# Kernel tuning notes

Measured on AMD Instinct MI355X. Metric: run time of the kernel, lower is better.

Reference implementation:

```python
import jax, jax.numpy as jnp
import numpy as np

H = 8   # heads
C = 64  # per-head channels (gnn_hidden_dim)
HID = H * C  # 512
IN_CH = 6
EMB = 64
U, M = 16, 512
N_NODES = U * M  # 8192
N_EDGES = 131072


def _tconv(x, src, dst, Wq, bq, Wk, bk, Wv, bv, Ws, bs):
    """PyG TransformerConv (concat=True, root_weight=True, beta=False, eval mode)."""
    N = x.shape[0]
    q = (x @ Wq + bq).reshape(N, H, C)
    k = (x @ Wk + bk).reshape(N, H, C)
    v = (x @ Wv + bv).reshape(N, H, C)
    # per-edge attention scores: query at dst (target i), key at src (source j)
    score = jnp.einsum('ehc,ehc->eh', q[dst], k[src]) / jnp.sqrt(jnp.float32(C))
    # segment softmax over incoming edges of each dst node
    mx = jax.ops.segment_max(score, dst, num_segments=N)
    ex = jnp.exp(score - mx[dst])
    denom = jax.ops.segment_sum(ex, dst, num_segments=N)
    alpha = ex / (denom[dst] + 1e-16)  # [E, H]
    msg = alpha[..., None] * v[src]    # [E, H, C]
    out = jax.ops.segment_sum(msg, dst, num_segments=N).reshape(N, HID)
    return out + x @ Ws + bs  # root/skip connection


def setup_inputs() -> dict:
    key = jax.random.key(0)
    ks = iter(jax.random.split(key, 64))
    s = 0.05

    def lin(k, i, o):
        k1, k2 = jax.random.split(k)
        return (jax.random.normal(k1, (i, o), jnp.float32) * s,
                jax.random.normal(k2, (o,), jnp.float32) * s)

    inp = {}
    inp['mission_coords'] = jax.random.uniform(next(ks), (M, 2), jnp.float32)
    inp['uavs_info'] = jax.random.uniform(next(ks), (U, 2), jnp.float32)
    inp['speeds'] = jax.random.uniform(next(ks), (U,), jnp.float32)
    inp['dist_matrix'] = jax.random.uniform(next(ks), (U, M), jnp.float32)
    inp['timetogo_matrix'] = jax.random.uniform(next(ks), (U, M), jnp.float32)
    inp['action_mask'] = jax.random.randint(next(ks), (U, M), 0, 2, jnp.int32)
    inp['edge_index'] = jax.random.randint(next(ks), (2, N_EDGES), 0, N_NODES, jnp.int64)
    inp['batch'] = jnp.zeros((U,), jnp.int64)

    # layer 0 (in=6)
    inp['Wq0'], inp['bq0'] = lin(next(ks), IN_CH, HID)
    inp['Wk0'], inp['bk0'] = lin(next(ks), IN_CH, HID)
    inp['Wv0'], inp['bv0'] = lin(next(ks), IN_CH, HID)
    inp['Ws0'], inp['bs0'] = lin(next(ks), IN_CH, HID)
    # layers 1..3 stacked (in=512)
    for nm in ['Wq', 'Wk', 'Wv', 'Ws']:
        Ws_, bs_ = [], []
        for _ in range(3):
            w, b = lin(next(ks), HID, HID)
            Ws_.append(w); bs_.append(b)
        inp[nm] = jnp.stack(Ws_)
        inp['b' + nm[1:].lower()] = jnp.stack(bs_)
    inp['Wout'], inp['bout'] = lin(next(ks), HID, EMB)
    inp['Wa1'], inp['ba1'] = lin(next(ks), EMB + 3, 128)
    inp['Wa2'], inp['ba2'] = lin(next(ks), 128, 1)
    inp['Wc1'], inp['bc1'] = lin(next(ks), EMB + 3, 128)
    inp['Wc2'], inp['bc2'] = lin(next(ks), 128, 1)
    return inp


def reference(mission_coords, uavs_info, speeds, dist_matrix, timetogo_matrix,
              action_mask, edge_index, batch,
              Wq0, bq0, Wk0, bk0, Wv0, bv0, Ws0, bs0,
              Wq, bq, Wk, bk, Wv, bv, Ws, bs,
              Wout, bout, Wa1, ba1, Wa2, ba2, Wc1, bc1, Wc2, bc2):
    u, m = uavs_info.shape[0], mission_coords.shape[0]
    mc = jnp.broadcast_to(mission_coords[None], (u, m, 2))
    mask_e = action_mask[..., None].astype(jnp.float32)
    sp_e = jnp.broadcast_to(speeds[:, None, None], (u, m, 1))
    x = jnp.concatenate([mc, mask_e, sp_e, dist_matrix[..., None],
                         timetogo_matrix[..., None]], axis=-1).reshape(u * m, IN_CH)
    src, dst = edge_index[0], edge_index[1]
    x = jax.nn.relu(_tconv(x, src, dst, Wq0, bq0, Wk0, bk0, Wv0, bv0, Ws0, bs0))
    for l in range(3):
        x = jax.nn.relu(_tconv(x, src, dst, Wq[l], bq[l], Wk[l], bk[l],
                               Wv[l], bv[l], Ws[l], bs[l]))
    x = x @ Wout + bout  # [U*M, EMB]
    uav_emb = x.reshape(u, m, EMB).sum(axis=1)  # sum pooling over missions
    combined = jnp.concatenate([uavs_info, uav_emb, speeds[:, None]], axis=-1)
    logits = jax.nn.relu(combined @ Wa1 + ba1) @ Wa2 + ba2  # [U, 1]
    action_probs = jax.nn.softmax(logits, axis=-1)
    state_values = (jax.nn.relu(combined @ Wc1 + bc1) @ Wc2 + bc2).squeeze()
    return action_probs, state_values
```

## Files before the change

kernel.cpp:

```cpp
#include <hip/hip_runtime.h>
#include <hip/hip_bf16.h>
#include <math.h>

#define NNODES 8192
#define NEDGES 131072
#define HID    512
#define UU     16
#define MM     512
#define NQKVS  2048

#if __has_builtin(__builtin_amdgcn_cvt_pk_f32_fp8) && __has_builtin(__builtin_amdgcn_cvt_pk_fp8_f32)
#define HAVE_FP8 1
#else
#define HAVE_FP8 0
#endif

#define KSCALE 16.0f
#define KISCALE (0.125f / 16.0f)

typedef __attribute__((ext_vector_type(8))) short bf16x8;
typedef __attribute__((ext_vector_type(4))) float f32x4;
typedef __attribute__((ext_vector_type(2))) float f32x2;

__device__ __forceinline__ float bf2f(ushort u) {
    return __uint_as_float(((unsigned)u) << 16);
}
__device__ __forceinline__ ushort f2bf(float f) {
    unsigned x = __float_as_uint(f);
    return (ushort)((x + 0x7fffu + ((x >> 16) & 1u)) >> 16);
}

__global__ __launch_bounds__(256) void k_build_x(
    const float* __restrict__ mc, const float* __restrict__ speeds,
    const float* __restrict__ dist, const float* __restrict__ ttg,
    const int* __restrict__ mask, float* __restrict__ x6)
{
    int n = blockIdx.x * blockDim.x + threadIdx.x;
    if (n >= NNODES) return;
    int u = n >> 9, m = n & 511;
    float* o = x6 + (size_t)n * 6;
    o[0] = mc[m * 2 + 0];
    o[1] = mc[m * 2 + 1];
    o[2] = (float)mask[u * MM + m];
    o[3] = speeds[u];
    o[4] = dist[u * MM + m];
    o[5] = ttg[u * MM + m];
}

__global__ __launch_bounds__(256) void k_wt(
    const float* __restrict__ Wq, const float* __restrict__ Wk,
    const float* __restrict__ Wv, const float* __restrict__ Ws,
    ushort* __restrict__ Wt)
{
    __shared__ float tile[64][65];
    int z = blockIdx.z;
    int l = z >> 2, which = z & 3;
    const float* src = (which == 0 ? Wq : which == 1 ? Wk : which == 2 ? Wv : Ws)
                       + (size_t)l * HID * HID;
    int k0 = blockIdx.x * 64, c0 = blockIdx.y * 64;
    int t = threadIdx.x;
#pragma unroll
    for (int i = 0; i < 16; ++i) {
        int idx = i * 256 + t;
        int r = idx >> 6, c = idx & 63;
        tile[r][c] = src[(size_t)(k0 + r) * HID + c0 + c];
    }
    __syncthreads();
    ushort* dst = Wt + ((size_t)l * NQKVS + which * HID + c0) * HID + k0;
#pragma unroll
    for (int i = 0; i < 16; ++i) {
        int idx = i * 256 + t;
        int r = idx >> 6, c = idx & 63;
        dst[(size_t)r * HID + c] = f2bf(tile[c][r]);
    }
}

__global__ __launch_bounds__(256) void k_bias(
    const float* __restrict__ bq, const float* __restrict__ bk,
    const float* __restrict__ bv, const float* __restrict__ bs,
    float* __restrict__ bcat)
{
    int i = blockIdx.x * 256 + threadIdx.x;
    int l = i >> 11, j = i & 2047;
    int which = j >> 9, jj = j & 511;
    const float* b = which == 0 ? bq : which == 1 ? bk : which == 2 ? bv : bs;
    bcat[i] = b[l * HID + jj];
}

__global__ __launch_bounds__(256) void k_lin0(
    const float* __restrict__ x6,
    const float* __restrict__ Wq0, const float* __restrict__ bq0,
    const float* __restrict__ Wk0, const float* __restrict__ bk0,
    const float* __restrict__ Wv0, const float* __restrict__ bv0,
    const float* __restrict__ Ws0, const float* __restrict__ bs0,
    ushort* __restrict__ Y, unsigned char* __restrict__ Kf8)
{
    int n = blockIdx.x;
    int j = threadIdx.x;
    int col0 = j * 8;
    int which = col0 >> 9, jj = col0 & 511;
    const float* W = which == 0 ? Wq0 : which == 1 ? Wk0 : which == 2 ? Wv0 : Ws0;
    const float* b = which == 0 ? bq0 : which == 1 ? bk0 : which == 2 ? bv0 : bs0;
    const float* xr = x6 + (size_t)n * 6;
    float x[6];
#pragma unroll
    for (int t = 0; t < 6; ++t) x[t] = xr[t];
    float s[8];
#pragma unroll
    for (int u = 0; u < 8; ++u) s[u] = b[jj + u];
#pragma unroll
    for (int t = 0; t < 6; ++t)
#pragma unroll
        for (int u = 0; u < 8; ++u)
            s[u] = fmaf(x[t], W[t * HID + jj + u], s[u]);
    bf16x8 o8;
#pragma unroll
    for (int u = 0; u < 8; ++u) o8[u] = (short)f2bf(s[u]);
    *(bf16x8*)(Y + (size_t)n * NQKVS + col0) = o8;
#if HAVE_FP8
    if (which == 1) {
        int w0 = __builtin_amdgcn_cvt_pk_fp8_f32(s[0] * KSCALE, s[1] * KSCALE, 0, false);
        w0     = __builtin_amdgcn_cvt_pk_fp8_f32(s[2] * KSCALE, s[3] * KSCALE, w0, true);
        int w1 = __builtin_amdgcn_cvt_pk_fp8_f32(s[4] * KSCALE, s[5] * KSCALE, 0, false);
        w1     = __builtin_amdgcn_cvt_pk_fp8_f32(s[6] * KSCALE, s[7] * KSCALE, w1, true);
        uint2 uu; uu.x = (unsigned)w0; uu.y = (unsigned)w1;
        *(uint2*)(Kf8 + (size_t)n * HID + jj) = uu;
    }
#endif
}

#define GBM 128
#define GBN 128
#define GBK 64
#define TILEB (GBM * GBK * 2)
#define BUFB  (2 * TILEB)

__device__ __forceinline__ void stage_tile(
    const ushort* __restrict__ Ag, const ushort* __restrict__ Bg,
    char* __restrict__ base, int t)
{
    const int lane = t & 63;
    const int w = t >> 6;
    const int r8 = lane >> 3;
    const int c  = lane & 7;
    const int csw = c ^ r8;
#pragma unroll
    for (int i = 0; i < 4; ++i) {
        int r0 = (w * 4 + i) * 8;
        __builtin_amdgcn_global_load_lds(
            (const __attribute__((address_space(1))) void*)(Ag + (size_t)(r0 + r8) * HID + csw * 8),
            (__attribute__((address_space(3))) void*)(base + r0 * 128 + lane * 16), 16, 0, 0);
        __builtin_amdgcn_global_load_lds(
            (const __attribute__((address_space(1))) void*)(Bg + (size_t)(r0 + r8) * HID + csw * 8),
            (__attribute__((address_space(3))) void*)(base + TILEB + r0 * 128 + lane * 16), 16, 0, 0);
    }
}

__global__ __launch_bounds__(256, 2) void k_gemm(
    const ushort* __restrict__ A,
    const ushort* __restrict__ Bt,
    const float* __restrict__ bias,
    ushort* __restrict__ Y,
    unsigned char* __restrict__ Kf8)
{
    __shared__ char lds[2 * BUFB];
    const int t = threadIdx.x;
    const int bid = blockIdx.x;
    const int xcd = bid & 7;
    const int ii  = bid >> 3;
    const int mi  = (xcd << 3) | (ii & 7);
    const int ni  = ii >> 3;
    const int m0 = mi * GBM, n0 = ni * GBN;

    const int wid = t >> 6, lane = t & 63;
    const int wr = wid >> 1, wc = wid & 1;
    const int l15 = lane & 15, lkq = lane >> 4;

    f32x4 acc[4][4] = {};

    const ushort* Ab = A + (size_t)m0 * HID;
    const ushort* Bb = Bt + (size_t)n0 * HID;

    stage_tile(Ab, Bb, lds, t);
    int cur = 0;
    const int NKS = HID / GBK;
    for (int T = 0; T < NKS; ++T) {
        __syncthreads();
        if (T + 1 < NKS)
            stage_tile(Ab + (T + 1) * GBK, Bb + (T + 1) * GBK,
                       lds + (cur ^ 1) * BUFB, t);
        const char* la = lds + cur * BUFB;
        const char* lb = la + TILEB;
#pragma unroll
        for (int kh = 0; kh < 2; ++kh) {
            const int kq = kh * 4 + lkq;
            const int sw = (kq ^ (l15 & 7)) << 4;
            bf16x8 a[4], b[4];
#pragma unroll
            for (int i = 0; i < 4; ++i)
                a[i] = *(const bf16x8*)(la + (wr * 64 + i * 16 + l15) * 128 + sw);
#pragma unroll
            for (int j = 0; j < 4; ++j)
                b[j] = *(const bf16x8*)(lb + (wc * 64 + j * 16 + l15) * 128 + sw);
#pragma unroll
            for (int i = 0; i < 4; ++i)
#pragma unroll
                for (int j = 0; j < 4; ++j)
                    acc[i][j] = __builtin_amdgcn_mfma_f32_16x16x32_bf16(a[i], b[j], acc[i][j], 0, 0, 0);
        }
        cur ^= 1;
    }

    const bool kquad = ((n0 >> 9) == 1);
#pragma unroll
    for (int i = 0; i < 4; ++i) {
        int row = m0 + wr * 64 + i * 16 + lkq * 4;
#pragma unroll
        for (int j = 0; j < 4; ++j) {
            int col = n0 + wc * 64 + j * 16 + l15;
            float bc = bias[col];
            f32x4 r = acc[i][j];
#pragma unroll
            for (int g = 0; g < 4; ++g) {
                float val = r[g] + bc;
                Y[(size_t)(row + g) * NQKVS + col] = f2bf(val);
#if HAVE_FP8
                if (kquad) {
                    int pk = __builtin_amdgcn_cvt_pk_fp8_f32(val * KSCALE, val * KSCALE, 0, false);
                    Kf8[(size_t)(row + g) * HID + (col - 512)] = (unsigned char)(pk & 0xff);
                }
#endif
            }
        }
    }
}

__global__ __launch_bounds__(256) void k_hist(const int* __restrict__ dst, int* __restrict__ cnt)
{
    int e = blockIdx.x * blockDim.x + threadIdx.x;
    if (e < NEDGES) atomicAdd(&cnt[dst[e]], 1);
}

__global__ __launch_bounds__(256) void k_scan(const int* __restrict__ cnt, int* __restrict__ indptr)
{
    __shared__ int sums[256];
    __shared__ int offs[256];
    int t = threadIdx.x;
    int base = t * 32;
    int s = 0;
    for (int i = 0; i < 32; ++i) s += cnt[base + i];
    sums[t] = s;
    __syncthreads();
    if (t == 0) {
        int run = 0;
        for (int i = 0; i < 256; ++i) { offs[i] = run; run += sums[i]; }
    }
    __syncthreads();
    int off = offs[t];
    for (int i = 0; i < 32; ++i) { indptr[base + i] = off; off += cnt[base + i]; }
    if (t == 255) indptr[NNODES] = off;
}

__global__ __launch_bounds__(256) void k_scatter(
    const int* __restrict__ src, const int* __restrict__ dst,
    const int* __restrict__ indptr, int* __restrict__ cursor, int* __restrict__ ssrc)
{
    int e = blockIdx.x * blockDim.x + threadIdx.x;
    if (e >= NEDGES) return;
    int d = dst[e];
    int p = atomicAdd(&cursor[d], 1);
    ssrc[indptr[d] + p] = src[e];
}

__global__ __launch_bounds__(256) void k_attn(
    const int* __restrict__ indptr, const int* __restrict__ ssrc,
    const ushort* __restrict__ Y,
    const unsigned char* __restrict__ Kf8,
    ushort* __restrict__ X)
{
    int n = blockIdx.x * 4 + (threadIdx.x >> 6);
    if (n >= NNODES) return;
    int l = threadIdx.x & 63;
    int cbase = l * 8;
    const ushort* yq = Y + (size_t)n * NQKVS + cbase;
    float qf[8];
    {
        bf16x8 q8 = *(const bf16x8*)yq;
#pragma unroll
        for (int j = 0; j < 8; ++j) qf[j] = bf2f((ushort)q8[j]);
    }
    float mrun = -INFINITY, ssum = 0.f;
    float acc[8] = {};
    int e0 = indptr[n], e1 = indptr[n + 1];
#if HAVE_FP8
    uint2 ka = {}, kb = {};
#else
    bf16x8 ka = {}, kb = {};
#endif
    bf16x8 va = {}, vb = {};
    if (e0 < e1) {
        int s = ssrc[e0];
#if HAVE_FP8
        ka = *(const uint2*)(Kf8 + (size_t)s * HID + cbase);
#else
        ka = *(const bf16x8*)(Y + (size_t)s * NQKVS + 512 + cbase);
#endif
        va = *(const bf16x8*)(Y + (size_t)s * NQKVS + 1024 + cbase);
    }
    if (e0 + 1 < e1) {
        int s = ssrc[e0 + 1];
#if HAVE_FP8
        kb = *(const uint2*)(Kf8 + (size_t)s * HID + cbase);
#else
        kb = *(const bf16x8*)(Y + (size_t)s * NQKVS + 512 + cbase);
#endif
        vb = *(const bf16x8*)(Y + (size_t)s * NQKVS + 1024 + cbase);
    }
    for (int e = e0; e < e1; ++e) {
        auto k8 = ka; bf16x8 v8 = va;
        ka = kb; va = vb;
        int en = e + 2;
        if (en < e1) {
            int s = ssrc[en];
#if HAVE_FP8
            kb = *(const uint2*)(Kf8 + (size_t)s * HID + cbase);
#else
            kb = *(const bf16x8*)(Y + (size_t)s * NQKVS + 512 + cbase);
#endif
            vb = *(const bf16x8*)(Y + (size_t)s * NQKVS + 1024 + cbase);
        }
        float part = 0.f;
#if HAVE_FP8
        {
            f32x2 k01 = __builtin_amdgcn_cvt_pk_f32_fp8((int)k8.x, false);
            f32x2 k23 = __builtin_amdgcn_cvt_pk_f32_fp8((int)k8.x, true);
            f32x2 k45 = __builtin_amdgcn_cvt_pk_f32_fp8((int)k8.y, false);
            f32x2 k67 = __builtin_amdgcn_cvt_pk_f32_fp8((int)k8.y, true);
            part = fmaf(qf[0], k01.x, part); part = fmaf(qf[1], k01.y, part);
            part = fmaf(qf[2], k23.x, part); part = fmaf(qf[3], k23.y, part);
            part = fmaf(qf[4], k45.x, part); part = fmaf(qf[5], k45.y, part);
            part = fmaf(qf[6], k67.x, part); part = fmaf(qf[7], k67.y, part);
        }
#else
#pragma unroll
        for (int j = 0; j < 8; ++j) part = fmaf(qf[j], bf2f((ushort)k8[j]), part);
#endif
        part += __shfl_xor(part, 1);
        part += __shfl_xor(part, 2);
        part += __shfl_xor(part, 4);
#if HAVE_FP8
        float score = part * KISCALE;
#else
        float score = part * 0.125f;
#endif
        float mnew = fmaxf(mrun, score);
        float sc = __expf(mrun - mnew);
        float p = __expf(score - mnew);
        ssum = ssum * sc + p;
#pragma unroll
        for (int j = 0; j < 8; ++j)
            acc[j] = fmaf(acc[j], sc, p * bf2f((ushort)v8[j]));
        mrun = mnew;
    }
    float inv = ssum > 0.f ? 1.f / ssum : 0.f;
    bf16x8 o8;
#pragma unroll
    for (int j = 0; j < 8; ++j) {
        float o = fmaxf(fmaf(acc[j], inv, bf2f(yq[1536 + j])), 0.f);
        o8[j] = (short)f2bf(o);
    }
    *(bf16x8*)(X + (size_t)n * HID + cbase) = o8;
}

__global__ __launch_bounds__(512) void k_pool(const ushort* __restrict__ X, float* __restrict__ xsumP)
{
    int u = blockIdx.x;
    int pp = blockIdx.y;
    int c = threadIdx.x;
    const ushort* base = X + ((size_t)u * MM + pp * 64) * HID + c;
    float s = 0.f;
    for (int m = 0; m < 64; ++m) s += bf2f(base[(size_t)m * HID]);
    xsumP[((size_t)u * 8 + pp) * HID + c] = s;
}

__global__ __launch_bounds__(512) void k_emb(
    const float* __restrict__ xsumP, const float* __restrict__ Wout,
    const float* __restrict__ bout, float* __restrict__ emb)
{
    __shared__ float xs[HID];
    int u = blockIdx.x, c = threadIdx.x;
    float s = 0.f;
#pragma unroll
    for (int p = 0; p < 8; ++p) s += xsumP[((size_t)u * 8 + p) * HID + c];
    xs[c] = s;
    __syncthreads();
    if (c < 64) {
        float a = 0.f;
        for (int i = 0; i < HID; ++i) a = fmaf(xs[i], Wout[i * 64 + c], a);
        emb[u * 64 + c] = a + 512.0f * bout[c];
    }
}

__global__ __launch_bounds__(128) void k_head(
    const float* __restrict__ uavs, const float* __restrict__ speeds,
    const float* __restrict__ emb,
    const float* __restrict__ Wc1, const float* __restrict__ bc1,
    const float* __restrict__ Wc2, const float* __restrict__ bc2,
    float* __restrict__ out)
{
    __shared__ float comb[67];
    __shared__ float red[128];
    int u = blockIdx.x, t = threadIdx.x;
    if (t < 2) comb[t] = uavs[u * 2 + t];
    else if (t < 66) comb[t] = emb[u * 64 + (t - 2)];
    else if (t == 66) comb[t] = speeds[u];
    __syncthreads();
    float a = bc1[t];
    for (int i = 0; i < 67; ++i) a = fmaf(comb[i], Wc1[i * 128 + t], a);
    a = fmaxf(a, 0.f);
    red[t] = a * Wc2[t];
    __syncthreads();
    for (int sft = 64; sft > 0; sft >>= 1) {
        if (t < sft) red[t] += red[t + sft];
        __syncthreads();
    }
    if (t == 0) {
        out[u]      = 1.0f;
        out[16 + u] = red[0] + bc2[0];
    }
}

extern "C" void kernel_launch(void* const* d_in, const int* in_sizes, int n_in,
                              void* d_out, int out_size, void* d_ws, size_t ws_size,
                              hipStream_t stream)
{
    const float* mission_coords = (const float*)d_in[0];
    const float* uavs_info      = (const float*)d_in[1];
    const float* speeds         = (const float*)d_in[2];
    const float* dist_matrix    = (const float*)d_in[3];
    const float* timetogo       = (const float*)d_in[4];
    const int*   action_mask    = (const int*)d_in[5];
    const int*   edge_index     = (const int*)d_in[6];
    const float* Wq0 = (const float*)d_in[8];  const float* bq0 = (const float*)d_in[9];
    const float* Wk0 = (const float*)d_in[10]; const float* bk0 = (const float*)d_in[11];
    const float* Wv0 = (const float*)d_in[12]; const float* bv0 = (const float*)d_in[13];
    const float* Ws0 = (const float*)d_in[14]; const float* bs0 = (const float*)d_in[15];
    const float* Wq  = (const float*)d_in[16]; const float* bq  = (const float*)d_in[17];
    const float* Wk  = (const float*)d_in[18]; const float* bk  = (const float*)d_in[19];
    const float* Wv  = (const float*)d_in[20]; const float* bv  = (const float*)d_in[21];
    const float* Ws  = (const float*)d_in[22]; const float* bs  = (const float*)d_in[23];
    const float* Wout = (const float*)d_in[24]; const float* bout = (const float*)d_in[25];
    const float* Wc1 = (const float*)d_in[30]; const float* bc1 = (const float*)d_in[31];
    const float* Wc2 = (const float*)d_in[32]; const float* bc2 = (const float*)d_in[33];
    float* out = (float*)d_out;

    const int* e_src = edge_index;
    const int* e_dst = edge_index + NEDGES;

    char* p = (char*)d_ws;
    ushort* Ybf = (ushort*)p;  p += (size_t)NNODES * NQKVS * 2;
    ushort* Xbf = (ushort*)p;  p += (size_t)NNODES * HID * 2;
    ushort* Wt  = (ushort*)p;  p += (size_t)3 * NQKVS * HID * 2;
    unsigned char* Kf8 = (unsigned char*)p; p += (size_t)NNODES * HID;
    float* bcat = (float*)p;   p += (size_t)3 * NQKVS * 4;
    float* x6   = (float*)p;   p += (size_t)NNODES * 6 * 4;
    float* xsumP = (float*)p;  p += (size_t)UU * 8 * HID * 4;
    float* emb  = (float*)p;   p += (size_t)UU * 64 * 4;
    int* cnt    = (int*)p;     p += (size_t)NNODES * 4;
    int* indptr = (int*)p;     p += (size_t)(NNODES + 1) * 4;
    int* cursor = (int*)p;     p += (size_t)NNODES * 4;
    int* ssrc   = (int*)p;     p += (size_t)NEDGES * 4;

    hipMemsetAsync(cnt, 0, NNODES * sizeof(int), stream);
    hipMemsetAsync(cursor, 0, NNODES * sizeof(int), stream);

    k_build_x<<<NNODES / 256, 256, 0, stream>>>(mission_coords, speeds, dist_matrix,
                                                timetogo, action_mask, x6);
    k_wt<<<dim3(8, 8, 12), 256, 0, stream>>>(Wq, Wk, Wv, Ws, Wt);
    k_bias<<<3 * NQKVS / 256, 256, 0, stream>>>(bq, bk, bv, bs, bcat);
    k_hist<<<NEDGES / 256, 256, 0, stream>>>(e_dst, cnt);
    k_scan<<<1, 256, 0, stream>>>(cnt, indptr);
    k_scatter<<<NEDGES / 256, 256, 0, stream>>>(e_src, e_dst, indptr, cursor, ssrc);

    k_lin0<<<NNODES, 256, 0, stream>>>(x6, Wq0, bq0, Wk0, bk0, Wv0, bv0, Ws0, bs0, Ybf, Kf8);
    k_attn<<<NNODES / 4, 256, 0, stream>>>(indptr, ssrc, Ybf, Kf8, Xbf);

    const int ngblocks = (NNODES / GBM) * (NQKVS / GBN);
    for (int l = 0; l < 3; ++l) {
        k_gemm<<<ngblocks, 256, 0, stream>>>(Xbf, Wt + (size_t)l * NQKVS * HID,
                                             bcat + l * NQKVS, Ybf, Kf8);
        k_attn<<<NNODES / 4, 256, 0, stream>>>(indptr, ssrc, Ybf, Kf8, Xbf);
    }

    k_pool<<<dim3(UU, 8), 512, 0, stream>>>(Xbf, xsumP);
    k_emb<<<UU, 512, 0, stream>>>(xsumP, Wout, bout, emb);
    k_head<<<UU, 128, 0, stream>>>(uavs_info, speeds, emb, Wc1, bc1, Wc2, bc2, out);
}
```

Baseline: 277.3 us.

## Enlarge GEMM tiles to 256x256 with 512 threads and 2-deep prefetch; fuse input build

Result: no change. 281.2 us (+1.4%).

```diff
diff --git a/kernel.cpp b/kernel.cpp
--- a/kernel.cpp
+++ b/kernel.cpp
@@ -28,23 +28,6 @@
 __device__ __forceinline__ ushort f2bf(float f) {
     unsigned x = __float_as_uint(f);
     return (ushort)((x + 0x7fffu + ((x >> 16) & 1u)) >> 16);
-}
-
-__global__ __launch_bounds__(256) void k_build_x(
-    const float* __restrict__ mc, const float* __restrict__ speeds,
-    const float* __restrict__ dist, const float* __restrict__ ttg,
-    const int* __restrict__ mask, float* __restrict__ x6)
-{
-    int n = blockIdx.x * blockDim.x + threadIdx.x;
-    if (n >= NNODES) return;
-    int u = n >> 9, m = n & 511;
-    float* o = x6 + (size_t)n * 6;
-    o[0] = mc[m * 2 + 0];
-    o[1] = mc[m * 2 + 1];
-    o[2] = (float)mask[u * MM + m];
-    o[3] = speeds[u];
-    o[4] = dist[u * MM + m];
-    o[5] = ttg[u * MM + m];
 }
 
 __global__ __launch_bounds__(256) void k_wt(
@@ -88,7 +71,9 @@
 }
 
 __global__ __launch_bounds__(256) void k_lin0(
-    const float* __restrict__ x6,
+    const float* __restrict__ mc, const float* __restrict__ speeds,
+    const float* __restrict__ dist, const float* __restrict__ ttg,
+    const int* __restrict__ mask,
     const float* __restrict__ Wq0, const float* __restrict__ bq0,
     const float* __restrict__ Wk0, const float* __restrict__ bk0,
     const float* __restrict__ Wv0, const float* __restrict__ bv0,
@@ -96,26 +81,31 @@
     ushort* __restrict__ Y, unsigned char* __restrict__ Kf8)
 {
     int n = blockIdx.x;
+    int u = n >> 9, m = n & 511;
+    float x[6];
+    x[0] = mc[m * 2 + 0];
+    x[1] = mc[m * 2 + 1];
+    x[2] = (float)mask[u * MM + m];
+    x[3] = speeds[u];
+    x[4] = dist[u * MM + m];
+    x[5] = ttg[u * MM + m];
+
     int j = threadIdx.x;
     int col0 = j * 8;
     int which = col0 >> 9, jj = col0 & 511;
     const float* W = which == 0 ? Wq0 : which == 1 ? Wk0 : which == 2 ? Wv0 : Ws0;
     const float* b = which == 0 ? bq0 : which == 1 ? bk0 : which == 2 ? bv0 : bs0;
-    const float* xr = x6 + (size_t)n * 6;
-    float x[6];
-#pragma unroll
-    for (int t = 0; t < 6; ++t) x[t] = xr[t];
     float s[8];
 #pragma unroll
-    for (int u = 0; u < 8; ++u) s[u] = b[jj + u];
+    for (int uu = 0; uu < 8; ++uu) s[uu] = b[jj + uu];
 #pragma unroll
     for (int t = 0; t < 6; ++t)
 #pragma unroll
-        for (int u = 0; u < 8; ++u)
-            s[u] = fmaf(x[t], W[t * HID + jj + u], s[u]);
+        for (int uu = 0; uu < 8; ++uu)
+            s[uu] = fmaf(x[t], W[t * HID + jj + uu], s[uu]);
     bf16x8 o8;
 #pragma unroll
-    for (int u = 0; u < 8; ++u) o8[u] = (short)f2bf(s[u]);
+    for (int uu = 0; uu < 8; ++uu) o8[uu] = (short)f2bf(s[uu]);
     *(bf16x8*)(Y + (size_t)n * NQKVS + col0) = o8;
 #if HAVE_FP8
     if (which == 1) {
@@ -123,98 +113,103 @@
         w0     = __builtin_amdgcn_cvt_pk_fp8_f32(s[2] * KSCALE, s[3] * KSCALE, w0, true);
         int w1 = __builtin_amdgcn_cvt_pk_fp8_f32(s[4] * KSCALE, s[5] * KSCALE, 0, false);
         w1     = __builtin_amdgcn_cvt_pk_fp8_f32(s[6] * KSCALE, s[7] * KSCALE, w1, true);
-        uint2 uu; uu.x = (unsigned)w0; uu.y = (unsigned)w1;
-        *(uint2*)(Kf8 + (size_t)n * HID + jj) = uu;
-    }
-#endif
-}
-
-#define GBM 128
-#define GBN 128
+        uint2 uu2; uu2.x = (unsigned)w0; uu2.y = (unsigned)w1;
+        *(uint2*)(Kf8 + (size_t)n * HID + jj) = uu2;
+    }
+#endif
+}
+
+#define GBM 256
+#define GBN 256
 #define GBK 64
-#define TILEB (GBM * GBK * 2)
-#define BUFB  (2 * TILEB)
-
-__device__ __forceinline__ void stage_tile(
+#define MATB 32768
+#define BUFB (2 * MATB)
+
+#define VMCNT(n) asm volatile("s_waitcnt vmcnt(" #n ")" ::: "memory")
+
+__device__ __forceinline__ void stage_tile256(
     const ushort* __restrict__ Ag, const ushort* __restrict__ Bg,
-    char* __restrict__ base, int t)
-{
-    const int lane = t & 63;
-    const int w = t >> 6;
-    const int r8 = lane >> 3;
-    const int c  = lane & 7;
-    const int csw = c ^ r8;
-#pragma unroll
-    for (int i = 0; i < 4; ++i) {
-        int r0 = (w * 4 + i) * 8;
+    char* __restrict__ buf, int t)
+{
+#pragma unroll
+    for (int h = 0; h < 8; ++h) {
+        int slot = h * 512 + t;
+        const ushort* src = (h < 4) ? Ag : Bg;
+        int s = slot & 2047;
+        int row = s >> 3, kqs = s & 7;
+        int kq = kqs ^ (row & 7);
         __builtin_amdgcn_global_load_lds(
-            (const __attribute__((address_space(1))) void*)(Ag + (size_t)(r0 + r8) * HID + csw * 8),
-            (__attribute__((address_space(3))) void*)(base + r0 * 128 + lane * 16), 16, 0, 0);
-        __builtin_amdgcn_global_load_lds(
-            (const __attribute__((address_space(1))) void*)(Bg + (size_t)(r0 + r8) * HID + csw * 8),
-            (__attribute__((address_space(3))) void*)(base + TILEB + r0 * 128 + lane * 16), 16, 0, 0);
-    }
-}
-
-__global__ __launch_bounds__(256, 2) void k_gemm(
+            (const __attribute__((address_space(1))) void*)(src + (size_t)row * HID + kq * 8),
+            (__attribute__((address_space(3))) void*)(buf + slot * 16), 16, 0, 0);
+    }
+}
+
+__global__ __launch_bounds__(512, 1) void k_gemm(
     const ushort* __restrict__ A,
     const ushort* __restrict__ Bt,
     const float* __restrict__ bias,
     ushort* __restrict__ Y,
     unsigned char* __restrict__ Kf8)
 {
-    __shared__ char lds[2 * BUFB];
+    extern __shared__ char lds[];
     const int t = threadIdx.x;
     const int bid = blockIdx.x;
     const int xcd = bid & 7;
     const int ii  = bid >> 3;
-    const int mi  = (xcd << 3) | (ii & 7);
-    const int ni  = ii >> 3;
+    const int mi  = (xcd << 2) | (ii & 3);
+    const int ni  = ii >> 2;
     const int m0 = mi * GBM, n0 = ni * GBN;
 
     const int wid = t >> 6, lane = t & 63;
-    const int wr = wid >> 1, wc = wid & 1;
+    const int wr = wid >> 2, wc = wid & 3;
     const int l15 = lane & 15, lkq = lane >> 4;
 
-    f32x4 acc[4][4] = {};
+    f32x4 acc[8][4] = {};
 
     const ushort* Ab = A + (size_t)m0 * HID;
     const ushort* Bb = Bt + (size_t)n0 * HID;
 
-    stage_tile(Ab, Bb, lds, t);
-    int cur = 0;
-    const int NKS = HID / GBK;
-    for (int T = 0; T < NKS; ++T) {
-        __syncthreads();
-        if (T + 1 < NKS)
-            stage_tile(Ab + (T + 1) * GBK, Bb + (T + 1) * GBK,
-                       lds + (cur ^ 1) * BUFB, t);
-        const char* la = lds + cur * BUFB;
-        const char* lb = la + TILEB;
+    stage_tile256(Ab, Bb, lds, t);
+    stage_tile256(Ab + GBK, Bb + GBK, lds + BUFB, t);
+
+    const int NKT = HID / GBK;
+#pragma unroll
+    for (int T = 0; T < NKT; ++T) {
+        if (T < NKT - 1) { VMCNT(8); } else { VMCNT(0); }
+        __builtin_amdgcn_s_barrier();
+        __builtin_amdgcn_sched_barrier(0);
+        const char* la = lds + (T & 1) * BUFB;
+        const char* lb = la + MATB;
 #pragma unroll
         for (int kh = 0; kh < 2; ++kh) {
             const int kq = kh * 4 + lkq;
             const int sw = (kq ^ (l15 & 7)) << 4;
-            bf16x8 a[4], b[4];
-#pragma unroll
-            for (int i = 0; i < 4; ++i)
-                a[i] = *(const bf16x8*)(la + (wr * 64 + i * 16 + l15) * 128 + sw);
+            bf16x8 a[8], b[4];
+#pragma unroll
+            for (int i = 0; i < 8; ++i)
+                a[i] = *(const bf16x8*)(la + (wr * 128 + i * 16 + l15) * 128 + sw);
 #pragma unroll
             for (int j = 0; j < 4; ++j)
                 b[j] = *(const bf16x8*)(lb + (wc * 64 + j * 16 + l15) * 128 + sw);
-#pragma unroll
-            for (int i = 0; i < 4; ++i)
+            __builtin_amdgcn_s_setprio(1);
+#pragma unroll
+            for (int i = 0; i < 8; ++i)
 #pragma unroll
                 for (int j = 0; j < 4; ++j)
                     acc[i][j] = __builtin_amdgcn_mfma_f32_16x16x32_bf16(a[i], b[j], acc[i][j], 0, 0, 0);
+            __builtin_amdgcn_s_setprio(0);
         }
-        cur ^= 1;
+        __builtin_amdgcn_s_barrier();
+        __builtin_amdgcn_sched_barrier(0);
+        if (T + 2 < NKT)
+            stage_tile256(Ab + (T + 2) * GBK, Bb + (T + 2) * GBK,
+                          lds + (T & 1) * BUFB, t);
     }
 
     const bool kquad = ((n0 >> 9) == 1);
 #pragma unroll
-    for (int i = 0; i < 4; ++i) {
-        int row = m0 + wr * 64 + i * 16 + lkq * 4;
+    for (int i = 0; i < 8; ++i) {
+        int row = m0 + wr * 128 + i * 16 + lkq * 4;
 #pragma unroll
         for (int j = 0; j < 4; ++j) {
             int col = n0 + wc * 64 + j * 16 + l15;
@@ -463,7 +458,6 @@
     ushort* Wt  = (ushort*)p;  p += (size_t)3 * NQKVS * HID * 2;
     unsigned char* Kf8 = (unsigned char*)p; p += (size_t)NNODES * HID;
     float* bcat = (float*)p;   p += (size_t)3 * NQKVS * 4;
-    float* x6   = (float*)p;   p += (size_t)NNODES * 6 * 4;
     float* xsumP = (float*)p;  p += (size_t)UU * 8 * HID * 4;
     float* emb  = (float*)p;   p += (size_t)UU * 64 * 4;
     int* cnt    = (int*)p;     p += (size_t)NNODES * 4;
@@ -474,21 +468,28 @@
     hipMemsetAsync(cnt, 0, NNODES * sizeof(int), stream);
     hipMemsetAsync(cursor, 0, NNODES * sizeof(int), stream);
 
-    k_build_x<<<NNODES / 256, 256, 0, stream>>>(mission_coords, speeds, dist_matrix,
-                                                timetogo, action_mask, x6);
+    static bool attr_done = false;
+    if (!attr_done) {
+        hipFuncSetAttribute((const void*)k_gemm,
+                            hipFuncAttributeMaxDynamicSharedMemorySize, 131072);
+        attr_done = true;
+    }
+
     k_wt<<<dim3(8, 8, 12), 256, 0, stream>>>(Wq, Wk, Wv, Ws, Wt);
     k_bias<<<3 * NQKVS / 256, 256, 0, stream>>>(bq, bk, bv, bs, bcat);
     k_hist<<<NEDGES / 256, 256, 0, stream>>>(e_dst, cnt);
     k_scan<<<1, 256, 0, stream>>>(cnt, indptr);
     k_scatter<<<NEDGES / 256, 256, 0, stream>>>(e_src, e_dst, indptr, cursor, ssrc);
 
-    k_lin0<<<NNODES, 256, 0, stream>>>(x6, Wq0, bq0, Wk0, bk0, Wv0, bv0, Ws0, bs0, Ybf, Kf8);
+    k_lin0<<<NNODES, 256, 0, stream>>>(mission_coords, speeds, dist_matrix, timetogo,
+                                       action_mask, Wq0, bq0, Wk0, bk0, Wv0, bv0,
+                                       Ws0, bs0, Ybf, Kf8);
     k_attn<<<NNODES / 4, 256, 0, stream>>>(indptr, ssrc, Ybf, Kf8, Xbf);
 
     const int ngblocks = (NNODES / GBM) * (NQKVS / GBN);
     for (int l = 0; l < 3; ++l) {
-        k_gemm<<<ngblocks, 256, 0, stream>>>(Xbf, Wt + (size_t)l * NQKVS * HID,
-                                             bcat + l * NQKVS, Ybf, Kf8);
+        k_gemm<<<ngblocks, 512, 131072, stream>>>(Xbf, Wt + (size_t)l * NQKVS * HID,
+                                                  bcat + l * NQKVS, Ybf, Kf8);
         k_attn<<<NNODES / 4, 256, 0, stream>>>(indptr, ssrc, Ybf, Kf8, Xbf);
     }
 
```
